# Optimization experiments

Measured on AMD Instinct MI355X. Metric: run time of the kernel, lower is better.

## Reference

```python
import jax, jax.numpy as jnp
import numpy as np
from jax import lax

REG = 0.1
REG_M = 0.001
N_ITER = 250  # POT default numItermax=1000 with early stopping; 250 fixed iters converges here
EPS = 1e-8

N_TOK = 4096
D_EMB = 2048


def _xavier_uniform(key, shape):
    fan_in, fan_out = shape
    bound = float(np.sqrt(6.0 / (fan_in + fan_out)))
    return jax.random.uniform(key, shape, jnp.float32, -bound, bound)


def setup_inputs() -> dict:
    key = jax.random.key(0)
    kx, ky, kd = jax.random.split(key, 3)
    X = jax.random.normal(kx, (N_TOK, D_EMB), jnp.float32)
    Y = jax.random.normal(ky, (N_TOK, D_EMB), jnp.float32)
    delta_ot = _xavier_uniform(kd, (N_TOK, N_TOK))
    return {"X": X, "Y": Y, "delta_ot": delta_ot}


def pairwise_cosine(X, Y):
    Xn = X / jnp.maximum(jnp.linalg.norm(X, axis=-1, keepdims=True), EPS)
    Yn = Y / jnp.maximum(jnp.linalg.norm(Y, axis=-1, keepdims=True), EPS)
    return Xn @ Yn.T  # [n, m]


def sinkhorn_unbalanced(M, reg, reg_m, n_iter):
    # POT ot.unbalanced.sinkhorn_unbalanced, KL-relaxed marginals, scaling form.
    n, m = M.shape
    a = jnp.full((n,), 1.0 / n, M.dtype)
    b = jnp.full((m,), 1.0 / m, M.dtype)
    K = jnp.exp(-M / reg)  # [n, m]
    fi = reg_m / (reg_m + reg)

    def step(carry, _):
        u, v = carry
        u = (a / (K @ v)) ** fi
        v = (b / (K.T @ u)) ** fi
        return (u, v), None

    (u, v), _ = lax.scan(step, (jnp.ones((n,), M.dtype), jnp.ones((m,), M.dtype)), None, length=n_iter)
    return u[:, None] * K * v[None, :]


def reference(X, Y, delta_ot):
    A = pairwise_cosine(X, Y)                      # [n, m]
    # OT weight computed on detached sim (sim.data in torch) -> stop_gradient
    M = -lax.stop_gradient(A)
    W = sinkhorn_unbalanced(M, REG, REG_M, N_ITER)  # [n, m], no grad
    T = A * W + delta_ot                            # [n, m]
    X_aligned = T @ X                               # [n, d] (requires m == n)
    return X_aligned
```

## Files before the change

kernel.cpp:

```cpp
#include <hip/hip_runtime.h>
#include <stdint.h>


typedef __attribute__((ext_vector_type(8))) __bf16 bf16x8;
typedef __attribute__((ext_vector_type(4))) float f32x4;
typedef __attribute__((ext_vector_type(8))) unsigned short ushort8;

#define N_TOK 4096
#define D_EMB 2048
#define FI 0.009900990099009901f
#define LOG2A (-12.0f)

__device__ __forceinline__ unsigned short f2bf(float f) {
  union { float f; uint32_t u; } c; c.f = f;
  uint32_t r = (c.u + 0x7FFFu + ((c.u >> 16) & 1u)) >> 16;
  return (unsigned short)r;
}
__device__ __forceinline__ float bf2f(unsigned short h) {
  union { uint32_t u; float f; } c; c.u = ((uint32_t)h) << 16;
  return c.f;
}
__device__ __forceinline__ float pow_fi_of(float s) {
  return exp2f(FI * (LOG2A - log2f(s)));
}

typedef const __attribute__((address_space(1))) unsigned int* as1_u32p;
typedef __attribute__((address_space(3))) unsigned int* as3_u32p;
__device__ __forceinline__ void gload16(const void* g, void* l) {
  __builtin_amdgcn_global_load_lds((as1_u32p)g, (as3_u32p)l, 16, 0, 0);
}

typedef __attribute__((address_space(3))) const char* lds_cp;
__device__ __forceinline__ bf16x8 ds_read16(lds_cp p) {
  bf16x8 r;
  asm volatile("ds_read_b128 %0, %1" : "=v"(r) : "v"(p));
  return r;
}

__device__ __forceinline__ void bar_raw() {
  asm volatile("s_barrier" ::: "memory");
}
__device__ __forceinline__ void sb0() { __builtin_amdgcn_sched_barrier(0); }
__device__ __forceinline__ void lgkm_wait4() {
  asm volatile("s_waitcnt lgkmcnt(4)" ::: "memory");
}
__device__ __forceinline__ void lgkm_wait0() {
  asm volatile("s_waitcnt lgkmcnt(0)" ::: "memory");
}

__global__ __launch_bounds__(256) void rownorm_bf16(const float* __restrict__ in,
                                                    unsigned short* __restrict__ out) {
  const int row = blockIdx.x;
  const int t = threadIdx.x;
  const float* r = in + (size_t)row * D_EMB;
  float4 a = *(const float4*)(r + t * 8);
  float4 b = *(const float4*)(r + t * 8 + 4);
  float s = a.x * a.x + a.y * a.y + a.z * a.z + a.w * a.w
          + b.x * b.x + b.y * b.y + b.z * b.z + b.w * b.w;
#pragma unroll
  for (int off = 32; off; off >>= 1) s += __shfl_xor(s, off);
  __shared__ float wsum[4];
  if ((t & 63) == 0) wsum[t >> 6] = s;
  __syncthreads();
  float tot = wsum[0] + wsum[1] + wsum[2] + wsum[3];
  float scale = 1.0f / fmaxf(sqrtf(tot), 1e-8f);
  ushort8 o;
  o[0] = f2bf(a.x * scale); o[1] = f2bf(a.y * scale);
  o[2] = f2bf(a.z * scale); o[3] = f2bf(a.w * scale);
  o[4] = f2bf(b.x * scale); o[5] = f2bf(b.y * scale);
  o[6] = f2bf(b.z * scale); o[7] = f2bf(b.w * scale);
  *(ushort8*)(out + (size_t)row * D_EMB + t * 8) = o;
}

__global__ __launch_bounds__(256) void transpose_f32_to_bf16(
    const float* __restrict__ in, unsigned short* __restrict__ out, int R, int C) {
  __shared__ float tile[32][33];
  const int bi = blockIdx.y * 32, bj = blockIdx.x * 32;
  const int tx = threadIdx.x, ty = threadIdx.y;
#pragma unroll
  for (int dy = 0; dy < 32; dy += 8)
    tile[ty + dy][tx] = in[(size_t)(bi + ty + dy) * C + bj + tx];
  __syncthreads();
#pragma unroll
  for (int dy = 0; dy < 32; dy += 8)
    out[(size_t)(bj + ty + dy) * R + bi + tx] = f2bf(tile[tx][ty + dy]);
}

__global__ __launch_bounds__(256, 1) void gemm256w4(
    const unsigned short* __restrict__ Amat, const unsigned short* __restrict__ Bmat,
    int ldA, int ldB, int nt, int ldC,
    unsigned short* __restrict__ outKbf, float* __restrict__ rsum) {
  __shared__ alignas(16) char smem[131072];
  const int t = threadIdx.x;
  const int l = t & 63;
  const int w = t >> 6;

  const int nwg = gridDim.x * gridDim.y;
  const int lin = blockIdx.y * gridDim.x + blockIdx.x;
  const int lin2 = (lin & 7) * (nwg >> 3) + (lin >> 3);
  const int bx = lin2 % gridDim.x;
  const int by = lin2 / gridDim.x;
  const int bM = by * 256;
  const int bN = bx * 256;
  const int wrow = w >> 1;
  const int wcol = w & 1;

  const unsigned short* Ag = Amat + (size_t)bM * ldA;
  const unsigned short* Bg = Bmat + (size_t)bN * ldB;

  const int st_row = w * 64 + (l >> 3);
  const int st_col = ((l & 7) ^ (l >> 3)) * 8;
  const int st_lds = w * 8192;

  const int rsw0 = (((l >> 4) + 0) ^ (l & 7)) * 16;
  const int rsw1 = (((l >> 4) + 4) ^ (l & 7)) * 16;
  const int arow = l & 15;

  auto stageA = [&](int k) {
    char* base = smem + (k & 1) * 32768 + st_lds;
    const unsigned short* g = Ag + (size_t)st_row * ldA + k * 64 + st_col;
#pragma unroll
    for (int i = 0; i < 8; ++i)
      gload16(g + (size_t)(i * 8) * ldA, base + i * 1024);
  };
  auto stageB = [&](int k) {
    char* base = smem + 65536 + (k & 1) * 32768 + st_lds;
    const unsigned short* g = Bg + (size_t)st_row * ldB + k * 64 + st_col;
#pragma unroll
    for (int i = 0; i < 8; ++i)
      gload16(g + (size_t)(i * 8) * ldB, base + i * 1024);
  };

  f32x4 acc[8][8] = {};

  stageA(0); stageB(0);
  asm volatile("s_waitcnt vmcnt(0)" ::: "memory");
  bar_raw();
  sb0();

  for (int k = 0; k < nt; ++k) {
    char* Abase = smem + (k & 1) * 32768;
    char* Bbase = smem + 65536 + (k & 1) * 32768;
    if (k + 1 < nt) { stageA(k + 1); stageB(k + 1); }

#pragma unroll
    for (int kk = 0; kk < 2; ++kk) {
      const int rsw = kk ? rsw1 : rsw0;
      bf16x8 af[8], bf[8];
#pragma unroll
      for (int m = 0; m < 8; ++m)
        af[m] = ds_read16((lds_cp)(Abase + (wrow * 128 + m * 16 + arow) * 128 + rsw));
#pragma unroll
      for (int n = 0; n < 8; ++n)
        bf[n] = ds_read16((lds_cp)(Bbase + (wcol * 128 + n * 16 + arow) * 128 + rsw));
      lgkm_wait0();
      sb0();
      __builtin_amdgcn_s_setprio(1);
#pragma unroll
      for (int m = 0; m < 8; ++m)
#pragma unroll
        for (int n = 0; n < 8; ++n)
          acc[m][n] = __builtin_amdgcn_mfma_f32_16x16x32_bf16(af[m], bf[n], acc[m][n], 0, 0, 0);
      __builtin_amdgcn_s_setprio(0);
      sb0();
    }

    asm volatile("s_waitcnt vmcnt(0)" ::: "memory");
    bar_raw();
    sb0();
  }

#pragma unroll
  for (int m = 0; m < 8; ++m) {
#pragma unroll
    for (int r = 0; r < 4; ++r) {
      const int i = bM + wrow * 128 + m * 16 + (l >> 4) * 4 + r;
      float rs = 0.0f;
#pragma unroll
      for (int n = 0; n < 8; ++n) {
        const int j = bN + wcol * 128 + n * 16 + (l & 15);
        const float kvf = __expf(10.0f * acc[m][n][r]);
        outKbf[(size_t)i * ldC + j] = f2bf(kvf);
        rs += kvf;
      }
      rs += __shfl_xor(rs, 1); rs += __shfl_xor(rs, 2);
      rs += __shfl_xor(rs, 4); rs += __shfl_xor(rs, 8);
      if ((l & 15) == 0) unsafeAtomicAdd(&rsum[i], rs);
    }
  }
}

template <int Q>
__device__ __forceinline__ void phase(char* Abase, int wrow, int arow, int rsw0,
                                      int rsw1, bf16x8 (&afc)[2][2],
                                      bf16x8 (&afn)[2][2], bf16x8 (&bfrag)[4][2],
                                      f32x4 (&acc)[8][4]) {
  sb0();
  if (Q < 3) {
#pragma unroll
    for (int mi = 0; mi < 2; ++mi) {
      const int row = wrow * 128 + ((Q + 1) * 2 + mi) * 16 + arow;
      afn[mi][0] = ds_read16((lds_cp)(Abase + row * 128 + rsw0));
      afn[mi][1] = ds_read16((lds_cp)(Abase + row * 128 + rsw1));
    }
    lgkm_wait4();
  } else {
    lgkm_wait0();
  }
  sb0();
  __builtin_amdgcn_s_setprio(1);
#pragma unroll
  for (int mi = 0; mi < 2; ++mi)
#pragma unroll
    for (int ni = 0; ni < 4; ++ni) {
      acc[Q * 2 + mi][ni] = __builtin_amdgcn_mfma_f32_16x16x32_bf16(
          afc[mi][0], bfrag[ni][0], acc[Q * 2 + mi][ni], 0, 0, 0);
      acc[Q * 2 + mi][ni] = __builtin_amdgcn_mfma_f32_16x16x32_bf16(
          afc[mi][1], bfrag[ni][1], acc[Q * 2 + mi][ni], 0, 0, 0);
    }
  __builtin_amdgcn_s_setprio(0);
}

__global__ __launch_bounds__(512, 2) void gemm256(
    const unsigned short* __restrict__ Amat, const unsigned short* __restrict__ Bmat,
    int ldA, int ldB, int nt, int kSlice, int ldC, float* __restrict__ outC) {
  __shared__ alignas(16) char smem[131072];
  const int t = threadIdx.x;
  const int l = t & 63;
  const int w = t >> 6;

  const int nwg = gridDim.x * gridDim.y;
  const int lin = blockIdx.y * gridDim.x + blockIdx.x;
  const int lin2 = (lin & 7) * (nwg >> 3) + (lin >> 3);
  const int bx = lin2 % gridDim.x;
  const int by = lin2 / gridDim.x;
  const int bM = by * 256;
  const int bN = bx * 256;
  const int wrow = w >> 2;
  const int wcol = w & 3;
  const int kOff = blockIdx.z * kSlice;

  const unsigned short* Ag = Amat + (size_t)bM * ldA + kOff;
  const unsigned short* Bg = Bmat + (size_t)bN * ldB + kOff;

  const int sl_r = w * 8 + (l >> 3);
  const int sl_c = ((l & 7) ^ (l >> 3)) * 8;
  const int s_lds = w * 1024;

  const int rsw0 = (((l >> 4) + 0) ^ (l & 7)) * 16;
  const int rsw1 = (((l >> 4) + 4) ^ (l & 7)) * 16;
  const int arow = l & 15;

  auto stage = [&](int k, int typ) {
    const int isA = typ >> 1;
    const int half = typ & 1;
    const unsigned short* G = isA ? Ag : Bg;
    const int ld = isA ? ldA : ldB;
    char* base = smem + (isA ? 0 : 65536) + (k & 1) * 32768 + half * 16384;
    const int gr = half * 128 + sl_r;
    const size_t gidx = (size_t)gr * ld + k * 64 + sl_c;
    gload16(G + gidx, base + s_lds);
    gload16(G + gidx + (size_t)64 * ld, base + 8192 + s_lds);
  };

  f32x4 acc[8][4] = {};
  bf16x8 bfrag[4][2];
  bf16x8 af_a[2][2], af_b[2][2];

  stage(0, 0); stage(0, 1); stage(0, 2); stage(0, 3);
  stage(1, 0); stage(1, 1);
  asm volatile("s_waitcnt vmcnt(4)" ::: "memory");
  bar_raw();
  sb0();

  for (int k = 0; k < nt; ++k) {
    char* Abase = smem + (k & 1) * 32768;
    char* Bbase = smem + 65536 + (k & 1) * 32768;
#pragma unroll
    for (int ni = 0; ni < 4; ++ni) {
      const int brow = wcol * 64 + ni * 16 + arow;
      bfrag[ni][0] = ds_read16((lds_cp)(Bbase + brow * 128 + rsw0));
      bfrag[ni][1] = ds_read16((lds_cp)(Bbase + brow * 128 + rsw1));
    }
#pragma unroll
    for (int mi = 0; mi < 2; ++mi) {
      const int row = wrow * 128 + mi * 16 + arow;
      af_a[mi][0] = ds_read16((lds_cp)(Abase + row * 128 + rsw0));
      af_a[mi][1] = ds_read16((lds_cp)(Abase + row * 128 + rsw1));
    }
    if (k + 1 < nt) { stage(k + 1, 2); stage(k + 1, 3); }

    phase<0>(Abase, wrow, arow, rsw0, rsw1, af_a, af_b, bfrag, acc);
    bar_raw();
    sb0();
    if (k + 2 < nt) stage(k + 2, 0);
    phase<1>(Abase, wrow, arow, rsw0, rsw1, af_b, af_a, bfrag, acc);
    if (k + 2 < nt) stage(k + 2, 1);
    phase<2>(Abase, wrow, arow, rsw0, rsw1, af_a, af_b, bfrag, acc);
    phase<3>(Abase, wrow, arow, rsw0, rsw1, af_b, af_a, bfrag, acc);

    sb0();
    if (k == nt - 2) asm volatile("s_waitcnt vmcnt(0)" ::: "memory");
    else if (k < nt - 2) asm volatile("s_waitcnt vmcnt(4)" ::: "memory");
    bar_raw();
    sb0();
  }

#pragma unroll
  for (int m = 0; m < 8; ++m)
#pragma unroll
    for (int n = 0; n < 4; ++n)
#pragma unroll
      for (int r = 0; r < 4; ++r) {
        const int i = bM + wrow * 128 + m * 16 + (l >> 4) * 4 + r;
        const int j = bN + wcol * 64 + n * 16 + (l & 15);
        unsafeAtomicAdd(&outC[(size_t)i * ldC + j], acc[m][n][r]);
      }
}

__global__ __launch_bounds__(256) void zero_small(float* p) {
  p[blockIdx.x * 256 + threadIdx.x] = 0.0f;
}

__global__ __launch_bounds__(256) void zero_f32(float4* p) {
  p[(size_t)blockIdx.x * 256 + threadIdx.x] = float4{0.f, 0.f, 0.f, 0.f};
}

__global__ __launch_bounds__(256) void colsum_u(
    const unsigned short* __restrict__ K, const float* __restrict__ rsum,
    float* __restrict__ s2) {
  __shared__ float part[8][256];
  const int j0 = blockIdx.x * 256;
  const int i0 = blockIdx.y * 128;
  const int c = (threadIdx.x & 31) * 8;
  const int rg = threadIdx.x >> 5;
  float acc[8] = {};
  for (int i = rg; i < 128; i += 8) {
    const float ui = pow_fi_of(rsum[i0 + i]);
    ushort8 kv = *(const ushort8*)(K + (size_t)(i0 + i) * N_TOK + j0 + c);
#pragma unroll
    for (int e = 0; e < 8; ++e) acc[e] += ui * bf2f(kv[e]);
  }
#pragma unroll
  for (int e = 0; e < 8; ++e) part[rg][c + e] = acc[e];
  __syncthreads();
  float s = 0.0f;
#pragma unroll
  for (int g = 0; g < 8; ++g) s += part[g][threadIdx.x];
  unsafeAtomicAdd(&s2[j0 + threadIdx.x], s);
}

__global__ __launch_bounds__(256) void build_T(
    const unsigned short* __restrict__ Kbf,
    const float* __restrict__ delta, const float* __restrict__ rsum,
    const float* __restrict__ s2, unsigned short* __restrict__ Tbf) {
  const size_t e = ((size_t)blockIdx.x * 256 + threadIdx.x) * 8;
  const int i = (int)(e >> 12);
  const int j = (int)(e & 4095);
  const float ui = pow_fi_of(rsum[i]);
  ushort8 kv = *(const ushort8*)(Kbf + e);
  float4 d0 = *(const float4*)(delta + e);
  float4 d1 = *(const float4*)(delta + e + 4);
  float4 t0 = *(const float4*)(s2 + j);
  float4 t1 = *(const float4*)(s2 + j + 4);
  float v0x = pow_fi_of(t0.x), v0y = pow_fi_of(t0.y), v0z = pow_fi_of(t0.z), v0w = pow_fi_of(t0.w);
  float v1x = pow_fi_of(t1.x), v1y = pow_fi_of(t1.y), v1z = pow_fi_of(t1.z), v1w = pow_fi_of(t1.w);
  ushort8 o;
  float k0 = bf2f(kv[0]), k1 = bf2f(kv[1]), k2 = bf2f(kv[2]), k3 = bf2f(kv[3]);
  float k4 = bf2f(kv[4]), k5 = bf2f(kv[5]), k6 = bf2f(kv[6]), k7 = bf2f(kv[7]);
  o[0] = f2bf(0.1f * __logf(k0) * (ui * k0 * v0x) + d0.x);
  o[1] = f2bf(0.1f * __logf(k1) * (ui * k1 * v0y) + d0.y);
  o[2] = f2bf(0.1f * __logf(k2) * (ui * k2 * v0z) + d0.z);
  o[3] = f2bf(0.1f * __logf(k3) * (ui * k3 * v0w) + d0.w);
  o[4] = f2bf(0.1f * __logf(k4) * (ui * k4 * v1x) + d1.x);
  o[5] = f2bf(0.1f * __logf(k5) * (ui * k5 * v1y) + d1.y);
  o[6] = f2bf(0.1f * __logf(k6) * (ui * k6 * v1z) + d1.z);
  o[7] = f2bf(0.1f * __logf(k7) * (ui * k7 * v1w) + d1.w);
  *(ushort8*)(Tbf + e) = o;
}

extern "C" void kernel_launch(void* const* d_in, const int* in_sizes, int n_in,
                              void* d_out, int out_size, void* d_ws, size_t ws_size,
                              hipStream_t stream) {
  const float* X = (const float*)d_in[0];
  const float* Y = (const float*)d_in[1];
  const float* delta = (const float*)d_in[2];
  float* out = (float*)d_out;
  uint8_t* ws = (uint8_t*)d_ws;

  const size_t SZ_NN_BF = (size_t)N_TOK * N_TOK * 2;
  const size_t SZ_ND_BF = (size_t)N_TOK * D_EMB * 2;

  unsigned short* K_bf = (unsigned short*)(ws);
  unsigned short* T_bf = (unsigned short*)(ws + SZ_NN_BF);
  unsigned short* Xn = (unsigned short*)(ws + 2 * SZ_NN_BF);
  unsigned short* XT = Xn;
  float* rsum = (float*)(ws + 2 * SZ_NN_BF + SZ_ND_BF);
  float* s2 = rsum + N_TOK;
  unsigned short* Yn = (unsigned short*)d_out;

  zero_small<<<32, 256, 0, stream>>>(rsum);
  rownorm_bf16<<<N_TOK, 256, 0, stream>>>(X, Xn);
  rownorm_bf16<<<N_TOK, 256, 0, stream>>>(Y, Yn);
  gemm256w4<<<dim3(16, 16, 1), 256, 0, stream>>>(
      Xn, Yn, D_EMB, D_EMB, D_EMB / 64, N_TOK, K_bf, rsum);
  zero_f32<<<(N_TOK * D_EMB / 4) / 256, 256, 0, stream>>>((float4*)out);
  transpose_f32_to_bf16<<<dim3(D_EMB / 32, N_TOK / 32), dim3(32, 8), 0, stream>>>(
      X, XT, N_TOK, D_EMB);
  colsum_u<<<dim3(16, 32), 256, 0, stream>>>(K_bf, rsum, s2);
  build_T<<<(N_TOK / 8) * (N_TOK / 256), 256, 0, stream>>>(K_bf, delta, rsum, s2, T_bf);
  gemm256<<<dim3(D_EMB / 256, N_TOK / 256, 2), 512, 0, stream>>>(
      T_bf, XT, N_TOK, N_TOK, D_EMB / 64, D_EMB, D_EMB, out);
}
```

Before: 242.9 us.

## Replace split-K 256x256 GEMM with full-K 256x128 tile and direct stores

The final T@X GEMM previously used 256x256 tiles with 2-way split-K, 512 threads, and atomic adds into a pre-zeroed output. It now uses 256x128 tiles over the full K range with 256 threads and a simpler double-buffered loop that loads all fragments and then issues the MFMAs. Results are written with plain stores, so the zero-fill kernel is removed. This trades the atomics and the zeroing pass for a longer K loop per block and less fine-grained overlap of LDS reads with MFMAs, at one block per CU.

```diff
diff --git a/kernel.cpp b/kernel.cpp
--- a/kernel.cpp
+++ b/kernel.cpp
@@ -41,9 +41,6 @@
   asm volatile("s_barrier" ::: "memory");
 }
 __device__ __forceinline__ void sb0() { __builtin_amdgcn_sched_barrier(0); }
-__device__ __forceinline__ void lgkm_wait4() {
-  asm volatile("s_waitcnt lgkmcnt(4)" ::: "memory");
-}
 __device__ __forceinline__ void lgkm_wait0() {
   asm volatile("s_waitcnt lgkmcnt(0)" ::: "memory");
 }
@@ -190,41 +187,10 @@
   }
 }
 
-template <int Q>
-__device__ __forceinline__ void phase(char* Abase, int wrow, int arow, int rsw0,
-                                      int rsw1, bf16x8 (&afc)[2][2],
-                                      bf16x8 (&afn)[2][2], bf16x8 (&bfrag)[4][2],
-                                      f32x4 (&acc)[8][4]) {
-  sb0();
-  if (Q < 3) {
-#pragma unroll
-    for (int mi = 0; mi < 2; ++mi) {
-      const int row = wrow * 128 + ((Q + 1) * 2 + mi) * 16 + arow;
-      afn[mi][0] = ds_read16((lds_cp)(Abase + row * 128 + rsw0));
-      afn[mi][1] = ds_read16((lds_cp)(Abase + row * 128 + rsw1));
-    }
-    lgkm_wait4();
-  } else {
-    lgkm_wait0();
-  }
-  sb0();
-  __builtin_amdgcn_s_setprio(1);
-#pragma unroll
-  for (int mi = 0; mi < 2; ++mi)
-#pragma unroll
-    for (int ni = 0; ni < 4; ++ni) {
-      acc[Q * 2 + mi][ni] = __builtin_amdgcn_mfma_f32_16x16x32_bf16(
-          afc[mi][0], bfrag[ni][0], acc[Q * 2 + mi][ni], 0, 0, 0);
-      acc[Q * 2 + mi][ni] = __builtin_amdgcn_mfma_f32_16x16x32_bf16(
-          afc[mi][1], bfrag[ni][1], acc[Q * 2 + mi][ni], 0, 0, 0);
-    }
-  __builtin_amdgcn_s_setprio(0);
-}
-
-__global__ __launch_bounds__(512, 2) void gemm256(
+__global__ __launch_bounds__(256, 1) void gemm_t2(
     const unsigned short* __restrict__ Amat, const unsigned short* __restrict__ Bmat,
-    int ldA, int ldB, int nt, int kSlice, int ldC, float* __restrict__ outC) {
-  __shared__ alignas(16) char smem[131072];
+    int ldA, int ldB, int nt, int ldC, float* __restrict__ outC) {
+  __shared__ alignas(16) char smem[98304];
   const int t = threadIdx.x;
   const int l = t & 63;
   const int w = t >> 6;
@@ -235,73 +201,73 @@
   const int bx = lin2 % gridDim.x;
   const int by = lin2 / gridDim.x;
   const int bM = by * 256;
-  const int bN = bx * 256;
-  const int wrow = w >> 2;
-  const int wcol = w & 3;
-  const int kOff = blockIdx.z * kSlice;
-
-  const unsigned short* Ag = Amat + (size_t)bM * ldA + kOff;
-  const unsigned short* Bg = Bmat + (size_t)bN * ldB + kOff;
-
-  const int sl_r = w * 8 + (l >> 3);
-  const int sl_c = ((l & 7) ^ (l >> 3)) * 8;
-  const int s_lds = w * 1024;
+  const int bN = bx * 128;
+  const int wrow = w >> 1;
+  const int wcol = w & 1;
+
+  const unsigned short* Ag = Amat + (size_t)bM * ldA;
+  const unsigned short* Bg = Bmat + (size_t)bN * ldB;
+
+  const int stA_row = w * 64 + (l >> 3);
+  const int st_col = ((l & 7) ^ (l >> 3)) * 8;
+  const int stA_lds = w * 8192;
+  const int stB_row = w * 32 + (l >> 3);
+  const int stB_lds = w * 4096;
 
   const int rsw0 = (((l >> 4) + 0) ^ (l & 7)) * 16;
   const int rsw1 = (((l >> 4) + 4) ^ (l & 7)) * 16;
   const int arow = l & 15;
 
-  auto stage = [&](int k, int typ) {
-    const int isA = typ >> 1;
-    const int half = typ & 1;
-    const unsigned short* G = isA ? Ag : Bg;
-    const int ld = isA ? ldA : ldB;
-    char* base = smem + (isA ? 0 : 65536) + (k & 1) * 32768 + half * 16384;
-    const int gr = half * 128 + sl_r;
-    const size_t gidx = (size_t)gr * ld + k * 64 + sl_c;
-    gload16(G + gidx, base + s_lds);
-    gload16(G + gidx + (size_t)64 * ld, base + 8192 + s_lds);
+  auto stageA = [&](int k) {
+    char* base = smem + (k & 1) * 32768 + stA_lds;
+    const unsigned short* g = Ag + (size_t)stA_row * ldA + k * 64 + st_col;
+#pragma unroll
+    for (int i = 0; i < 8; ++i)
+      gload16(g + (size_t)(i * 8) * ldA, base + i * 1024);
   };
+  auto stageB = [&](int k) {
+    char* base = smem + 65536 + (k & 1) * 16384 + stB_lds;
+    const unsigned short* g = Bg + (size_t)stB_row * ldB + k * 64 + st_col;
+#pragma unroll
+    for (int i = 0; i < 4; ++i)
+      gload16(g + (size_t)(i * 8) * ldB, base + i * 1024);
+  };
 
   f32x4 acc[8][4] = {};
-  bf16x8 bfrag[4][2];
-  bf16x8 af_a[2][2], af_b[2][2];
-
-  stage(0, 0); stage(0, 1); stage(0, 2); stage(0, 3);
-  stage(1, 0); stage(1, 1);
-  asm volatile("s_waitcnt vmcnt(4)" ::: "memory");
+
+  stageA(0); stageB(0);
+  asm volatile("s_waitcnt vmcnt(0)" ::: "memory");
   bar_raw();
   sb0();
 
   for (int k = 0; k < nt; ++k) {
     char* Abase = smem + (k & 1) * 32768;
-    char* Bbase = smem + 65536 + (k & 1) * 32768;
-#pragma unroll
-    for (int ni = 0; ni < 4; ++ni) {
-      const int brow = wcol * 64 + ni * 16 + arow;
-      bfrag[ni][0] = ds_read16((lds_cp)(Bbase + brow * 128 + rsw0));
-      bfrag[ni][1] = ds_read16((lds_cp)(Bbase + brow * 128 + rsw1));
+    char* Bbase = smem + 65536 + (k & 1) * 16384;
+    if (k + 1 < nt) { stageA(k + 1); stageB(k + 1); }
+
+#pragma unroll
+    for (int kk = 0; kk < 2; ++kk) {
+      const int rsw = kk ? rsw1 : rsw0;
+      bf16x8 af[8], bf[4];
+#pragma unroll
+      for (int m = 0; m < 8; ++m)
+        af[m] = ds_read16((lds_cp)(Abase + (wrow * 128 + m * 16 + arow) * 128 + rsw));
+#pragma unroll
+      for (int n = 0; n < 4; ++n)
+        bf[n] = ds_read16((lds_cp)(Bbase + (wcol * 64 + n * 16 + arow) * 128 + rsw));
+      lgkm_wait0();
+      sb0();
+      __builtin_amdgcn_s_setprio(1);
+#pragma unroll
+      for (int m = 0; m < 8; ++m)
+#pragma unroll
+        for (int n = 0; n < 4; ++n)
+          acc[m][n] = __builtin_amdgcn_mfma_f32_16x16x32_bf16(af[m], bf[n], acc[m][n], 0, 0, 0);
+      __builtin_amdgcn_s_setprio(0);
+      sb0();
     }
-#pragma unroll
-    for (int mi = 0; mi < 2; ++mi) {
-      const int row = wrow * 128 + mi * 16 + arow;
-      af_a[mi][0] = ds_read16((lds_cp)(Abase + row * 128 + rsw0));
-      af_a[mi][1] = ds_read16((lds_cp)(Abase + row * 128 + rsw1));
-    }
-    if (k + 1 < nt) { stage(k + 1, 2); stage(k + 1, 3); }
-
-    phase<0>(Abase, wrow, arow, rsw0, rsw1, af_a, af_b, bfrag, acc);
-    bar_raw();
-    sb0();
-    if (k + 2 < nt) stage(k + 2, 0);
-    phase<1>(Abase, wrow, arow, rsw0, rsw1, af_b, af_a, bfrag, acc);
-    if (k + 2 < nt) stage(k + 2, 1);
-    phase<2>(Abase, wrow, arow, rsw0, rsw1, af_a, af_b, bfrag, acc);
-    phase<3>(Abase, wrow, arow, rsw0, rsw1, af_b, af_a, bfrag, acc);
-
-    sb0();
-    if (k == nt - 2) asm volatile("s_waitcnt vmcnt(0)" ::: "memory");
-    else if (k < nt - 2) asm volatile("s_waitcnt vmcnt(4)" ::: "memory");
+
+    asm volatile("s_waitcnt vmcnt(0)" ::: "memory");
     bar_raw();
     sb0();
   }
@@ -314,16 +280,12 @@
       for (int r = 0; r < 4; ++r) {
         const int i = bM + wrow * 128 + m * 16 + (l >> 4) * 4 + r;
         const int j = bN + wcol * 64 + n * 16 + (l & 15);
-        unsafeAtomicAdd(&outC[(size_t)i * ldC + j], acc[m][n][r]);
+        outC[(size_t)i * ldC + j] = acc[m][n][r];
       }
 }
 
 __global__ __launch_bounds__(256) void zero_small(float* p) {
   p[blockIdx.x * 256 + threadIdx.x] = 0.0f;
-}
-
-__global__ __launch_bounds__(256) void zero_f32(float4* p) {
-  p[(size_t)blockIdx.x * 256 + threadIdx.x] = float4{0.f, 0.f, 0.f, 0.f};
 }
 
 __global__ __launch_bounds__(256) void colsum_u(
@@ -404,11 +366,10 @@
   rownorm_bf16<<<N_TOK, 256, 0, stream>>>(Y, Yn);
   gemm256w4<<<dim3(16, 16, 1), 256, 0, stream>>>(
       Xn, Yn, D_EMB, D_EMB, D_EMB / 64, N_TOK, K_bf, rsum);
-  zero_f32<<<(N_TOK * D_EMB / 4) / 256, 256, 0, stream>>>((float4*)out);
   transpose_f32_to_bf16<<<dim3(D_EMB / 32, N_TOK / 32), dim3(32, 8), 0, stream>>>(
       X, XT, N_TOK, D_EMB);
   colsum_u<<<dim3(16, 32), 256, 0, stream>>>(K_bf, rsum, s2);
   build_T<<<(N_TOK / 8) * (N_TOK / 256), 256, 0, stream>>>(K_bf, delta, rsum, s2, T_bf);
-  gemm256<<<dim3(D_EMB / 256, N_TOK / 256, 2), 512, 0, stream>>>(
-      T_bf, XT, N_TOK, N_TOK, D_EMB / 64, D_EMB, D_EMB, out);
-}
+  gemm_t2<<<dim3(16, 16, 1), 256, 0, stream>>>(
+      T_bf, XT, N_TOK, N_TOK, N_TOK / 64, D_EMB, out);
+}
```

Result: faster. 208.3 us (-14.2%).
